# Performance work log

Measured on AMD Instinct MI355X. Metric: run time of the kernel, lower is better.

The kernel has to match this reference:

```python
import jax, jax.numpy as jnp
import numpy as np

EPS = 1e-6
TOP_K = 3
GELU_MASK_TOL = 1e-6


def _dwconv(x, w, b):
    # x: [N, C, H, W], w: [C, 1, 7, 7] depthwise (groups = C)
    y = jax.lax.conv_general_dilated(
        x, w, window_strides=(1, 1), padding=[(3, 3), (3, 3)],
        dimension_numbers=('NCHW', 'OIHW', 'NCHW'),
        feature_group_count=w.shape[0])
    if b is not None:
        y = y + b[None, :, None, None]
    return y


def _topk_pi(ph):
    # indices of top-3 |phi| along the source axis (last dim), as int16 pointers
    return jax.lax.top_k(jnp.abs(ph), TOP_K)[1].astype(jnp.int16)


def setup_inputs() -> dict:
    key = jax.random.key(0)
    ks = jax.random.split(key, 9)
    B, C, H, W, S = 1, 96, 40, 40, 100
    signal = jax.random.normal(ks[0], (B, C, H, W), jnp.float32)
    phi = jax.random.normal(ks[1], (B, C, H, W, S), jnp.float32)
    beta = jax.random.normal(ks[2], (B, C, H, W, 1), jnp.float32)
    dw_w = jax.random.normal(ks[3], (C, 1, 7, 7), jnp.float32) * 0.05
    dw_b = jax.random.normal(ks[4], (C,), jnp.float32) * 0.05
    ln_w = jnp.ones((C,), jnp.float32)
    ln_b = jnp.zeros((C,), jnp.float32)
    w1 = jax.random.normal(ks[5], (4 * C, C), jnp.float32) * (1.0 / np.sqrt(C))
    b1 = jax.random.normal(ks[6], (4 * C,), jnp.float32) * 0.05
    w2 = jax.random.normal(ks[7], (C, 4 * C), jnp.float32) * (1.0 / np.sqrt(4 * C))
    b2 = jax.random.normal(ks[8], (C,), jnp.float32) * 0.05
    gamma = jnp.full((C,), 0.01, jnp.float32)  # layer_scale_init_value
    return dict(signal=signal, phi=phi, beta=beta, dw_w=dw_w, dw_b=dw_b,
                ln_w=ln_w, ln_b=ln_b, w1=w1, b1=b1, w2=w2, b2=b2, gamma=gamma)


def reference(signal, phi, beta, dw_w, dw_b, ln_w, ln_b, w1, b1, w2, b2, gamma):
    B, C, H, W = signal.shape
    S = phi.shape[-1]

    # ---- HoloConv2d_v3 (depthwise 7x7, p=3) ----
    s = _dwconv(signal, dw_w, dw_b)
    bt = _dwconv(beta[..., 0], dw_w, dw_b)[..., None]
    ph = jnp.transpose(phi, (0, 4, 1, 2, 3)).reshape(B * S, C, H, W)
    ph = _dwconv(ph, dw_w, None).reshape(B, S, C, H, W).transpose(0, 2, 3, 4, 1)
    pi = _topk_pi(ph)

    # permute to channels_last: [B,H,W,C(,S)]
    s = s.transpose(0, 2, 3, 1)
    bt = bt.transpose(0, 2, 3, 1, 4)
    ph = ph.transpose(0, 2, 3, 1, 4)

    # ---- HoloLayerNorm_v3 (channels_last) ----
    u = s.mean(-1, keepdims=True)
    var = jnp.var(s, axis=-1, keepdims=True)  # unbiased=False
    inv = 1.0 / jnp.sqrt(var + EPS)
    scale = ln_w * inv           # [B,H,W,C]
    shift = ln_b - u * scale
    s = (s - u) * inv * ln_w + ln_b
    bt = bt * scale[..., None] + shift[..., None]
    ph = ph * scale[..., None]

    # ---- pwconv1: dim -> 4*dim (phi without bias) ----
    s = jnp.einsum('bhwc,oc->bhwo', s, w1) + b1
    bt = (jnp.einsum('bhwc,oc->bhwo', bt[..., 0], w1) + b1)[..., None]
    ph = jnp.einsum('bhwcs,oc->bhwos', ph, w1)
    pi = _topk_pi(ph)

    # ---- HoloGELU_v3 (exact erf GELU + safe ratio) ----
    g = jax.nn.gelu(s, approximate=False)
    m = jnp.abs(s) > GELU_MASK_TOL
    ratio = jnp.where(m, g / jnp.where(m, s, 1.0), 0.0)
    bt = bt * ratio[..., None]
    ph = ph * ratio[..., None]
    s = g

    # ---- pwconv2: 4*dim -> dim ----
    s = jnp.einsum('bhwo,co->bhwc', s, w2) + b2
    bt = (jnp.einsum('bhwo,co->bhwc', bt[..., 0], w2) + b2)[..., None]
    ph = jnp.einsum('bhwos,co->bhwcs', ph, w2)
    pi = _topk_pi(ph)

    # ---- layer scale ----
    s = s * gamma
    bt = bt * gamma[..., None]
    ph = ph * gamma[..., None]

    # back to channels_first + residual (pi has no residual)
    s = s.transpose(0, 3, 1, 2) + signal
    bt = bt.transpose(0, 3, 1, 2, 4) + beta
    ph = ph.transpose(0, 3, 1, 2, 4) + phi
    pi = pi.transpose(0, 3, 1, 2, 4)
    return s, ph, bt, pi
```

## Files before the change

### kernel.cpp

```cpp
#include <hip/hip_runtime.h>
#include <math.h>

#define Cc 96
#define C4 384
#define Hh 40
#define Ww 40
#define Pp 1600
#define Ss 100
#define S4 25
#define Nn 9216

#define OFF_S  0
#define OFF_PH 153600
#define OFF_BT 15513600
#define OFF_PI 15667200

#define WS_W1T   0
#define WS_W2T   36864
#define WS_RATIO 73728
#define WS_SC    WS_RATIO
#define WS_BC    (WS_RATIO + 153600)
#define WS_SCALE 688128
#define WS_RH    841728
#define WS_RM    1148928
#define WS_RL    1456128
#define WS_GH    1763328
#define WS_GM    3532800
#define WS_GL    5302272
#define WS_T     7071744
#define CHUNK    640
#define WS_NEED_CHUNK (WS_T + CHUNK*Nn)
#define WS_NEED_FULL  (WS_T + Pp*Nn)

typedef __attribute__((ext_vector_type(8))) short bf16x8_t;
typedef __attribute__((ext_vector_type(4))) float f32x4_t;

__device__ inline float4 f4fma(float4 a, float w, float4 b){
  a.x += w*b.x; a.y += w*b.y; a.z += w*b.z; a.w += w*b.w; return a;
}
__device__ inline unsigned short bf16_rne(float x){
  unsigned int u = __float_as_uint(x);
  return (unsigned short)((u + 0x7fffu + ((u>>16)&1u)) >> 16);
}
__device__ inline float bf16_to_f(unsigned short h){
  return __uint_as_float(((unsigned int)h)<<16);
}
__device__ inline void gload16(const void* g, void* l){
  __builtin_amdgcn_global_load_lds(
    (const __attribute__((address_space(1))) void*)g,
    (__attribute__((address_space(3))) void*)l, 16, 0, 0);
}

__global__ __launch_bounds__(256) void k0_transpose(const float* __restrict__ w1,
    const float* __restrict__ w2, float* __restrict__ ws){
  int idx = blockIdx.x*256 + threadIdx.x;
  if (idx < C4*Cc){
    int o = idx/Cc, c = idx%Cc;
    ws[WS_W1T + c*C4 + o] = w1[idx];
    int c2 = idx/C4, o2 = idx%C4;
    ws[WS_W2T + o2*Cc + c2] = w2[idx];
  }
}

__global__ __launch_bounds__(256) void k0g3(const float* __restrict__ w2,
    float* __restrict__ wsm){
  int i = blockIdx.x;
  int base = blockIdx.y * (Cc*C4/8);
  unsigned short* gh = (unsigned short*)(wsm + WS_GH);
  unsigned short* gm = (unsigned short*)(wsm + WS_GM);
  unsigned short* gl = (unsigned short*)(wsm + WS_GL);
  for (int k = threadIdx.x; k < Cc*C4/8; k += 256){
    int idx = base + k;
    int j = idx / C4, o = idx % C4;
    float g = w2[i*C4 + o] * wsm[WS_W1T + j*C4 + o];
    unsigned short h = bf16_rne(g);           float fh = bf16_to_f(h);
    unsigned short m = bf16_rne(g - fh);      float fm2 = bf16_to_f(m);
    unsigned short lo = bf16_rne(g - fh - fm2);
    size_t off = ((size_t)i*Cc + j)*C4 + o;
    gh[off] = h; gm[off] = m; gl[off] = lo;
  }
}

__global__ __launch_bounds__(256) void k1a_dwconv(const float* __restrict__ signal,
    const float* __restrict__ beta, const float* __restrict__ dw_w,
    const float* __restrict__ dw_b, float* __restrict__ ws){
  int c = blockIdx.x;
  int pp = blockIdx.y*256 + threadIdx.x;
  if (pp >= Pp) return;
  int h = pp / Ww, w = pp % Ww;
  float wk[49];
  #pragma unroll
  for (int i=0; i<49; i++) wk[i] = dw_w[c*49 + i];
  const float* sb = signal + (size_t)c*Pp;
  const float* bb = beta   + (size_t)c*Pp;
  float sc = 0.f, btc = 0.f;
  #pragma unroll
  for (int ky=0; ky<7; ky++){
    int y = h + ky - 3;
    if (y >= 0 && y < Hh){
      #pragma unroll
      for (int kx=0; kx<7; kx++){
        int x = w + kx - 3;
        if (x >= 0 && x < Ww){
          float wv = wk[ky*7+kx];
          sc  = fmaf(wv, sb[y*Ww + x], sc);
          btc = fmaf(wv, bb[y*Ww + x], btc);
        }
      }
    }
  }
  float b = dw_b[c];
  ws[WS_SC + (size_t)c*Pp + pp] = sc + b;
  ws[WS_BC + (size_t)c*Pp + pp] = btc + b;
}

__global__ __launch_bounds__(384) void k1_scalar(
    const float* __restrict__ signal, const float* __restrict__ beta,
    const float* __restrict__ ln_w, const float* __restrict__ ln_b,
    const float* __restrict__ b1, const float* __restrict__ b2,
    const float* __restrict__ gamma, float* __restrict__ ws,
    float* __restrict__ out){
  int p = blockIdx.x, t = threadIdx.x;
  int g = t / 96, c = t - g*96;
  __shared__ float scp[4][96], btp[4][96];
  __shared__ float sl[Cc], bl[Cc], g1[C4], g2[C4], red[2];

  float sc = 0.f, btc = 0.f;
  if (t < 96){
    sc  = ws[WS_SC + (size_t)t*Pp + p];
    btc = ws[WS_BC + (size_t)t*Pp + p];
    scp[0][t] = sc;
  }
  __syncthreads();
  if (t < 64){
    float x = scp[0][t] + (t < 32 ? scp[0][64+t] : 0.f);
    #pragma unroll
    for (int off=32; off>0; off>>=1) x += __shfl_xor(x, off);
    if (t == 0) red[0] = x * (1.f/Cc);
  }
  __syncthreads();
  float u = red[0];
  if (t < 96){ float d = sc - u; scp[1][t] = d*d; }
  __syncthreads();
  if (t < 64){
    float x = scp[1][t] + (t < 32 ? scp[1][64+t] : 0.f);
    #pragma unroll
    for (int off=32; off>0; off>>=1) x += __shfl_xor(x, off);
    if (t == 0) red[1] = x * (1.f/Cc);
  }
  __syncthreads();
  float inv = 1.0f / sqrtf(red[1] + 1e-6f);
  if (t < 96){
    float scl = ln_w[t] * inv;
    ws[WS_SCALE + p*Cc + t] = scl;
    sl[t] = (sc - u)*inv*ln_w[t] + ln_b[t];
    bl[t] = btc*scl + (ln_b[t] - u*scl);
  }
  __syncthreads();
  {
    float a = b1[t], e = b1[t];
    const float* wp = ws + WS_W1T + t;
    for (int cc=0; cc<Cc; cc++){
      float wv = wp[cc*C4];
      a = fmaf(wv, sl[cc], a);
      e = fmaf(wv, bl[cc], e);
    }
    float x = a;
    float gg = 0.5f*x*(1.f + erff(x*0.70710678118654752f));
    float r = (fabsf(x) > 1e-6f) ? gg/x : 0.f;
    unsigned short* rh = (unsigned short*)(ws + WS_RH);
    unsigned short* rm = (unsigned short*)(ws + WS_RM);
    unsigned short* rl = (unsigned short*)(ws + WS_RL);
    unsigned short hh = bf16_rne(r);          float fh = bf16_to_f(hh);
    unsigned short hm = bf16_rne(r - fh);     float fm2 = bf16_to_f(hm);
    unsigned short hl = bf16_rne(r - fh - fm2);
    rh[(size_t)p*C4 + t] = hh;
    rm[(size_t)p*C4 + t] = hm;
    rl[(size_t)p*C4 + t] = hl;
    g1[t] = gg;
    g2[t] = e*r;
  }
  __syncthreads();
  {
    float pa = 0.f, pb = 0.f;
    const float* w2p = ws + WS_W2T + (size_t)(g*96)*Cc + c;
    for (int oo=0; oo<96; oo++){
      float wv = w2p[(size_t)oo*Cc];
      pa = fmaf(wv, g1[g*96+oo], pa);
      pb = fmaf(wv, g2[g*96+oo], pb);
    }
    scp[g][c] = pa; btp[g][c] = pb;
  }
  __syncthreads();
  if (t < 96){
    float acc  = scp[0][t]+scp[1][t]+scp[2][t]+scp[3][t] + b2[t];
    float accb = btp[0][t]+btp[1][t]+btp[2][t]+btp[3][t] + b2[t];
    float gm = gamma[t];
    out[OFF_S  + t*Pp + p] = acc*gm  + signal[t*Pp + p];
    out[OFF_BT + t*Pp + p] = accb*gm + beta[t*Pp + p];
  }
}

__global__ __launch_bounds__(384) void k1_fallback(
    const float* __restrict__ signal, const float* __restrict__ beta,
    const float* __restrict__ dw_w, const float* __restrict__ dw_b,
    const float* __restrict__ ln_w, const float* __restrict__ ln_b,
    const float* __restrict__ b1, const float* __restrict__ b2,
    const float* __restrict__ gamma, float* __restrict__ ws,
    float* __restrict__ out){
  int p = blockIdx.x, t = threadIdx.x;
  int h = p / Ww, w = p % Ww;
  int g = t / 96, c = t - g*96;
  __shared__ float scp[4][96], btp[4][96];
  __shared__ float sl[Cc], bl[Cc], g1[C4], g2[C4], red[2];
  float scpart = 0.f, btpart = 0.f;
  {
    const float* wk = dw_w + c*49;
    const float* sb = signal + c*Pp;
    const float* bb = beta   + c*Pp;
    #pragma unroll
    for (int kk=0; kk<2; kk++){
      int ky = g + kk*4;
      if (ky < 7){
        int y = h + ky - 3;
        if (y >= 0 && y < Hh){
          #pragma unroll
          for (int kx=0; kx<7; kx++){
            int x = w + kx - 3;
            if (x >= 0 && x < Ww){
              float wv = wk[ky*7+kx];
              scpart  += wv * sb[y*Ww + x];
              btpart  += wv * bb[y*Ww + x];
            }
          }
        }
      }
    }
  }
  scp[g][c] = scpart; btp[g][c] = btpart;
  __syncthreads();
  float sc = 0.f, btc = 0.f;
  if (t < 96){
    sc  = scp[0][t]+scp[1][t]+scp[2][t]+scp[3][t] + dw_b[t];
    btc = btp[0][t]+btp[1][t]+btp[2][t]+btp[3][t] + dw_b[t];
    scp[0][t] = sc;
  }
  __syncthreads();
  if (t < 64){
    float x = scp[0][t] + (t < 32 ? scp[0][64+t] : 0.f);
    #pragma unroll
    for (int off=32; off>0; off>>=1) x += __shfl_xor(x, off);
    if (t == 0) red[0] = x * (1.f/Cc);
  }
  __syncthreads();
  float u = red[0];
  if (t < 96){ float d = sc - u; scp[1][t] = d*d; }
  __syncthreads();
  if (t < 64){
    float x = scp[1][t] + (t < 32 ? scp[1][64+t] : 0.f);
    #pragma unroll
    for (int off=32; off>0; off>>=1) x += __shfl_xor(x, off);
    if (t == 0) red[1] = x * (1.f/Cc);
  }
  __syncthreads();
  float inv = 1.0f / sqrtf(red[1] + 1e-6f);
  if (t < 96){
    float scl = ln_w[t] * inv;
    ws[WS_SCALE + p*Cc + t] = scl;
    sl[t] = (sc - u)*inv*ln_w[t] + ln_b[t];
    bl[t] = btc*scl + (ln_b[t] - u*scl);
  }
  __syncthreads();
  {
    float a = b1[t], e = b1[t];
    const float* wp = ws + WS_W1T + t;
    for (int cc=0; cc<Cc; cc++){
      float wv = wp[cc*C4];
      a = fmaf(wv, sl[cc], a);
      e = fmaf(wv, bl[cc], e);
    }
    float x = a;
    float gg = 0.5f*x*(1.f + erff(x*0.70710678118654752f));
    float r = (fabsf(x) > 1e-6f) ? gg/x : 0.f;
    ws[WS_RATIO + p*C4 + t] = r;
    g1[t] = gg;
    g2[t] = e*r;
  }
  __syncthreads();
  {
    float pa = 0.f, pb = 0.f;
    const float* w2p = ws + WS_W2T + (size_t)(g*96)*Cc + c;
    for (int oo=0; oo<96; oo++){
      float wv = w2p[(size_t)oo*Cc];
      pa = fmaf(wv, g1[g*96+oo], pa);
      pb = fmaf(wv, g2[g*96+oo], pb);
    }
    scp[g][c] = pa; btp[g][c] = pb;
  }
  __syncthreads();
  if (t < 96){
    float acc  = scp[0][t]+scp[1][t]+scp[2][t]+scp[3][t] + b2[t];
    float accb = btp[0][t]+btp[1][t]+btp[2][t]+btp[3][t] + b2[t];
    float gm = gamma[t];
    out[OFF_S  + t*Pp + p] = acc*gm  + signal[t*Pp + p];
    out[OFF_BT + t*Pp + p] = accb*gm + beta[t*Pp + p];
  }
}

#define STRIP 10
__global__ __launch_bounds__(256) void k2_phiconv(const float* __restrict__ phi,
    const float* __restrict__ dw_w, const float* __restrict__ wsc,
    float* __restrict__ out){
  int c = blockIdx.x;
  int task = blockIdx.y*256 + threadIdx.x;
  if (task >= Ww*S4) return;
  int w = task / S4, ss = task % S4;
  int s0 = blockIdx.z * STRIP;
  float wk[49];
  #pragma unroll
  for (int i=0; i<49; i++) wk[i] = dw_w[c*49 + i];
  const float* base = phi + (size_t)c*Pp*Ss + ss*4;
  float* ob = out + OFF_PH + (size_t)c*Pp*Ss + (size_t)w*Ss + ss*4;
  float4 z = make_float4(0.f,0.f,0.f,0.f);
  float4 a0=z,a1=z,a2=z,a3=z,a4=z,a5=z,a6=z;
  #pragma unroll
  for (int rr=0; rr<STRIP+6; rr++){
    int r = s0 - 3 + rr;
    if (r >= 0 && r < Hh){
      #pragma unroll
      for (int kx=0; kx<7; kx++){
        int x = w + kx - 3;
        if (x >= 0 && x < Ww){
          float4 in4 = *(const float4*)(base + ((size_t)r*Ww + x)*Ss);
          a0 = f4fma(a0, wk[42+kx], in4);
          a1 = f4fma(a1, wk[35+kx], in4);
          a2 = f4fma(a2, wk[28+kx], in4);
          a3 = f4fma(a3, wk[21+kx], in4);
          a4 = f4fma(a4, wk[14+kx], in4);
          a5 = f4fma(a5, wk[ 7+kx], in4);
          a6 = f4fma(a6, wk[ 0+kx], in4);
        }
      }
    }
    int hrow = r - 3;
    if (hrow >= s0 && hrow < s0 + STRIP && hrow < Hh){
      float scv = wsc[WS_SCALE + (hrow*Ww + w)*Cc + c];
      float4 o; o.x=a0.x*scv; o.y=a0.y*scv; o.z=a0.z*scv; o.w=a0.w*scv;
      *(float4*)(ob + (size_t)hrow*Ww*Ss) = o;
    }
    a0=a1; a1=a2; a2=a3; a3=a4; a4=a5; a5=a6; a6=z;
  }
}

__global__ __launch_bounds__(256) void k3g(float* __restrict__ wsm, int P0, int mtiles){
  const unsigned short* rH = (const unsigned short*)(wsm + WS_RH);
  const unsigned short* rM = (const unsigned short*)(wsm + WS_RM);
  const unsigned short* rL = (const unsigned short*)(wsm + WS_RL);
  const unsigned short* gH = (const unsigned short*)(wsm + WS_GH);
  const unsigned short* gM = (const unsigned short*)(wsm + WS_GM);
  const unsigned short* gL = (const unsigned short*)(wsm + WS_GL);
  float* tc = wsm + WS_T;

  int nblk = mtiles*72;
  int bid = blockIdx.x;
  int swz = (bid & 7)*(nblk>>3) + (bid >> 3);
  int mt = swz % mtiles, nt = swz / mtiles;
  int m0 = mt*128, n0 = nt*128;
  int t = threadIdx.x, w = t >> 6, l = t & 63;

  __shared__ __align__(16) unsigned short lds[6*4096];
  unsigned short *AH = lds,        *AM = lds+4096,  *AL = lds+8192,
                 *BH = lds+12288,  *BM = lds+16384, *BL = lds+20480;

  f32x4_t acc[4][4];
  #pragma unroll
  for (int i=0;i<4;i++)
    #pragma unroll
    for (int j=0;j<4;j++) acc[i][j] = (f32x4_t){0.f,0.f,0.f,0.f};

  int wm = (w >> 1)*64, wn = (w & 1)*64;
  int srow = w*32 + (l>>2), sbyte = (l&3)*16;
  int pA0 = P0 + m0 + srow;      if (pA0 > Pp-1) pA0 = Pp-1;
  int pA1 = P0 + m0 + srow + 16; if (pA1 > Pp-1) pA1 = Pp-1;
  int nB0 = n0 + srow, nB1 = nB0 + 16;
  int kgb = (l>>4)*16;
  int lr  = l & 15;

  for (int ks=0; ks<12; ks++){
    int k0 = ks*32;
    size_t a0o = ((size_t)pA0*C4 + k0)*2 + sbyte;
    size_t a1o = ((size_t)pA1*C4 + k0)*2 + sbyte;
    size_t b0o = ((size_t)nB0*C4 + k0)*2 + sbyte;
    size_t b1o = ((size_t)nB1*C4 + k0)*2 + sbyte;
    gload16((const char*)rH + a0o, (char*)AH + w*2048);
    gload16((const char*)rH + a1o, (char*)AH + w*2048 + 1024);
    gload16((const char*)rM + a0o, (char*)AM + w*2048);
    gload16((const char*)rM + a1o, (char*)AM + w*2048 + 1024);
    gload16((const char*)rL + a0o, (char*)AL + w*2048);
    gload16((const char*)rL + a1o, (char*)AL + w*2048 + 1024);
    gload16((const char*)gH + b0o, (char*)BH + w*2048);
    gload16((const char*)gH + b1o, (char*)BH + w*2048 + 1024);
    gload16((const char*)gM + b0o, (char*)BM + w*2048);
    gload16((const char*)gM + b1o, (char*)BM + w*2048 + 1024);
    gload16((const char*)gL + b0o, (char*)BL + w*2048);
    gload16((const char*)gL + b1o, (char*)BL + w*2048 + 1024);
    asm volatile("s_waitcnt vmcnt(0)" ::: "memory");
    __syncthreads();

    bf16x8_t aH[4], aM[4], aL[4], bHf[4], bMf[4], bLf[4];
    #pragma unroll
    for (int f=0; f<4; f++){
      int ra = (wm + f*16 + lr)*64 + kgb;
      int rb = (wn + f*16 + lr)*64 + kgb;
      aH[f]  = *(const bf16x8_t*)((const char*)AH + ra);
      aM[f]  = *(const bf16x8_t*)((const char*)AM + ra);
      aL[f]  = *(const bf16x8_t*)((const char*)AL + ra);
      bHf[f] = *(const bf16x8_t*)((const char*)BH + rb);
      bMf[f] = *(const bf16x8_t*)((const char*)BM + rb);
      bLf[f] = *(const bf16x8_t*)((const char*)BL + rb);
    }
    #pragma unroll
    for (int i=0;i<4;i++)
      #pragma unroll
      for (int j=0;j<4;j++){
        acc[i][j] = __builtin_amdgcn_mfma_f32_16x16x32_bf16(aH[i], bHf[j], acc[i][j], 0,0,0);
        acc[i][j] = __builtin_amdgcn_mfma_f32_16x16x32_bf16(aH[i], bMf[j], acc[i][j], 0,0,0);
        acc[i][j] = __builtin_amdgcn_mfma_f32_16x16x32_bf16(aM[i], bHf[j], acc[i][j], 0,0,0);
        acc[i][j] = __builtin_amdgcn_mfma_f32_16x16x32_bf16(aH[i], bLf[j], acc[i][j], 0,0,0);
        acc[i][j] = __builtin_amdgcn_mfma_f32_16x16x32_bf16(aM[i], bMf[j], acc[i][j], 0,0,0);
        acc[i][j] = __builtin_amdgcn_mfma_f32_16x16x32_bf16(aL[i], bHf[j], acc[i][j], 0,0,0);
      }
    __syncthreads();
  }

  #pragma unroll
  for (int fm=0; fm<4; fm++){
    int prow = P0 + m0 + wm + fm*16 + (l>>4)*4;
    #pragma unroll
    for (int fn=0; fn<4; fn++){
      int ncol = n0 + wn + fn*16 + lr;
      #pragma unroll
      for (int r=0; r<4; r++){
        int p = prow + r;
        if (p < Pp) tc[(size_t)(p - P0)*Nn + ncol] = acc[fm][fn][r];
      }
    }
  }
}

#define PHP 100
__global__ __launch_bounds__(512,6) void k3b_apply(const float* __restrict__ phi,
    const float* __restrict__ gamma, const float* __restrict__ wsm,
    float* __restrict__ out, int P0){
  int p = P0 + blockIdx.x, t = threadIdx.x;
  __shared__ float lp[9700];
  const float* Tg = wsm + WS_T + (size_t)blockIdx.x*Nn;
  for (int q=t; q < Cc*S4; q += 512){
    int cc = q/S4, sg = q%S4;
    *(float4*)&lp[cc*PHP + sg*4] =
      *(const float4*)(out + OFF_PH + (size_t)cc*Pp*Ss + (size_t)p*Ss + sg*4);
  }
  __syncthreads();
  int w = t >> 6, l = t & 63;
  int wu = __builtin_amdgcn_readfirstlane(w);
  const float* Tb = Tg + (size_t)wu*12*Cc;
  float2 acc[12];
  #pragma unroll
  for (int k=0;k<12;k++) acc[k] = make_float2(0.f,0.f);
  if (l < 50){
    for (int cb=0; cb<Cc; cb+=4){
      float2 pv0 = *(float2*)&lp[(cb+0)*PHP + l*2];
      float2 pv1 = *(float2*)&lp[(cb+1)*PHP + l*2];
      float2 pv2 = *(float2*)&lp[(cb+2)*PHP + l*2];
      float2 pv3 = *(float2*)&lp[(cb+3)*PHP + l*2];
      #pragma unroll
      for (int k=0;k<12;k++){
        float4 tv = *(const float4*)(Tb + k*Cc + cb);
        acc[k].x = fmaf(tv.x, pv0.x, acc[k].x);
        acc[k].y = fmaf(tv.x, pv0.y, acc[k].y);
        acc[k].x = fmaf(tv.y, pv1.x, acc[k].x);
        acc[k].y = fmaf(tv.y, pv1.y, acc[k].y);
        acc[k].x = fmaf(tv.z, pv2.x, acc[k].x);
        acc[k].y = fmaf(tv.z, pv2.y, acc[k].y);
        acc[k].x = fmaf(tv.w, pv3.x, acc[k].x);
        acc[k].y = fmaf(tv.w, pv3.y, acc[k].y);
      }
    }
    #pragma unroll
    for (int k=0;k<12;k++){
      int c = wu*12 + k;
      float gm = gamma[c];
      float2 pv = *(const float2*)(phi + (size_t)c*Pp*Ss + (size_t)p*Ss + l*2);
      float2 res;
      res.x = fmaf(acc[k].x, gm, pv.x); res.y = fmaf(acc[k].y, gm, pv.y);
      *(float2*)(out + OFF_PH + (size_t)c*Pp*Ss + (size_t)p*Ss + l*2) = res;
      acc[k].x = fabsf(acc[k].x); acc[k].y = fabsf(acc[k].y);
    }
  }
  __syncthreads();
  if (l < 50){
    #pragma unroll
    for (int k=0;k<12;k++){
      int c = wu*12 + k;
      lp[(l*2+0)*97 + c] = acc[k].x;
      lp[(l*2+1)*97 + c] = acc[k].y;
    }
  }
  __syncthreads();
  if (t < Cc){
    float v1=-1.f, v2=-1.f, v3=-1.f; int i1=0, i2=0, i3=0;
    for (int s=0; s<Ss; s++){
      float v = lp[s*97 + t];
      if (v > v1){ v3=v2;i3=i2; v2=v1;i2=i1; v1=v;i1=s; }
      else if (v > v2){ v3=v2;i3=i2; v2=v;i2=s; }
      else if (v > v3){ v3=v;i3=s; }
    }
    float* po = out + OFF_PI + (size_t)t*Pp*3 + (size_t)p*3;
    po[0] = (float)i1; po[1] = (float)i2; po[2] = (float)i3;
  }
}

__global__ __launch_bounds__(256) void k3_heavy(const float* __restrict__ phi,
     const float* __restrict__ w1, const float* __restrict__ gamma,
     const float* __restrict__ ws, float* __restrict__ out){
  int p = blockIdx.x, t = threadIdx.x;
  __shared__ float r_lds[C4];
  __shared__ float phc[Cc*Ss];
  __shared__ float Tm[Cc*Cc];
  __shared__ float pool[Cc*Ss];
  float* A1  = pool;
  float* W2s = pool + 32*Cc;
  r_lds[t] = ws[WS_RATIO + p*C4 + t];
  if (t < C4-256) r_lds[256+t] = ws[WS_RATIO + p*C4 + 256 + t];
  __syncthreads();
  for (int q=t; q < Cc*S4; q += 256){
    int cc = q/S4, s = q%S4;
    *(float4*)(phc + cc*Ss + s*4) =
      *(const float4*)(out + OFF_PH + (size_t)cc*Pp*Ss + (size_t)p*Ss + s*4);
  }
  int ti = t >> 4, tj = t & 15;
  float acc[6][6];
  #pragma unroll
  for (int k=0;k<6;k++)
    #pragma unroll
    for (int m=0;m<6;m++) acc[k][m] = 0.f;
  for (int ot=0; ot<C4; ot+=32){
    __syncthreads();
    for (int q=t; q < 32*Cc; q += 256){
      int oo = q/Cc, cc = q%Cc;
      A1[q]  = w1[(size_t)(ot+oo)*Cc + cc] * r_lds[ot+oo];
      W2s[q] = ws[WS_W2T + (ot+oo)*Cc + cc];
    }
    __syncthreads();
    #pragma unroll 4
    for (int oo=0; oo<32; oo++){
      float av[6], bv[6];
      #pragma unroll
      for (int m=0;m<6;m++) av[m] = A1[oo*Cc + tj*6 + m];
      #pragma unroll
      for (int k=0;k<6;k++) bv[k] = W2s[oo*Cc + ti*6 + k];
      #pragma unroll
      for (int k=0;k<6;k++)
        #pragma unroll
        for (int m=0;m<6;m++) acc[k][m] += bv[k]*av[m];
    }
  }
  __syncthreads();
  #pragma unroll
  for (int k=0;k<6;k++)
    #pragma unroll
    for (int m=0;m<6;m++) Tm[(ti*6+k)*Cc + tj*6 + m] = acc[k][m];
  __syncthreads();
  float* absb = pool;
  for (int q=t; q < 24*S4; q += 256){
    int cb = q/S4, s = q%S4;
    float4 z = make_float4(0.f,0.f,0.f,0.f);
    float4 o0=z, o1=z, o2=z, o3=z;
    const float* t0 = Tm + (cb*4+0)*Cc;
    const float* t1 = Tm + (cb*4+1)*Cc;
    const float* t2 = Tm + (cb*4+2)*Cc;
    const float* t3 = Tm + (cb*4+3)*Cc;
    for (int cc=0; cc<Cc; cc++){
      float4 ph4 = *(const float4*)(phc + cc*Ss + s*4);
      o0 = f4fma(o0, t0[cc], ph4);
      o1 = f4fma(o1, t1[cc], ph4);
      o2 = f4fma(o2, t2[cc], ph4);
      o3 = f4fma(o3, t3[cc], ph4);
    }
    float4 ov[4] = {o0,o1,o2,o3};
    #pragma unroll
    for (int k=0;k<4;k++){
      int c = cb*4 + k;
      float g = gamma[c];
      float4 pv = *(const float4*)(phi + (size_t)c*Pp*Ss + (size_t)p*Ss + s*4);
      float4 res;
      res.x = ov[k].x*g + pv.x; res.y = ov[k].y*g + pv.y;
      res.z = ov[k].z*g + pv.z; res.w = ov[k].w*g + pv.w;
      *(float4*)(out + OFF_PH + (size_t)c*Pp*Ss + (size_t)p*Ss + s*4) = res;
      absb[c*Ss + s*4 + 0] = fabsf(ov[k].x);
      absb[c*Ss + s*4 + 1] = fabsf(ov[k].y);
      absb[c*Ss + s*4 + 2] = fabsf(ov[k].z);
      absb[c*Ss + s*4 + 3] = fabsf(ov[k].w);
    }
  }
  __syncthreads();
  if (t < Cc){
    float v1=-1.f, v2=-1.f, v3=-1.f; int i1=0, i2=0, i3=0;
    for (int s=0; s<Ss; s++){
      float v = absb[t*Ss + s];
      if (v > v1){ v3=v2;i3=i2; v2=v1;i2=i1; v1=v;i1=s; }
      else if (v > v2){ v3=v2;i3=i2; v2=v;i2=s; }
      else if (v > v3){ v3=v;i3=s; }
    }
    float* po = out + OFF_PI + (size_t)t*Pp*3 + (size_t)p*3;
    po[0] = (float)i1; po[1] = (float)i2; po[2] = (float)i3;
  }
}

extern "C" void kernel_launch(void* const* d_in, const int* in_sizes, int n_in,
                              void* d_out, int out_size, void* d_ws, size_t ws_size,
                              hipStream_t stream){
  const float* signal = (const float*)d_in[0];
  const float* phi    = (const float*)d_in[1];
  const float* beta   = (const float*)d_in[2];
  const float* dw_w   = (const float*)d_in[3];
  const float* dw_b   = (const float*)d_in[4];
  const float* ln_w   = (const float*)d_in[5];
  const float* ln_b   = (const float*)d_in[6];
  const float* w1     = (const float*)d_in[7];
  const float* b1     = (const float*)d_in[8];
  const float* w2     = (const float*)d_in[9];
  const float* b2     = (const float*)d_in[10];
  const float* gamma  = (const float*)d_in[11];
  float* out = (float*)d_out;
  float* ws  = (float*)d_ws;

  size_t wsf = ws_size / 4;
  hipLaunchKernelGGL(k0_transpose, dim3(144), dim3(256), 0, stream, w1, w2, ws);

  if (wsf >= (size_t)WS_NEED_CHUNK){
    hipLaunchKernelGGL(k1a_dwconv, dim3(96,7), dim3(256), 0, stream,
                       signal, beta, dw_w, dw_b, ws);
    hipLaunchKernelGGL(k1_scalar, dim3(Pp), dim3(384), 0, stream,
                       signal, beta, ln_w, ln_b, b1, b2, gamma, ws, out);
  } else {
    hipLaunchKernelGGL(k1_fallback, dim3(Pp), dim3(384), 0, stream,
                       signal, beta, dw_w, dw_b, ln_w, ln_b, b1, b2, gamma, ws, out);
  }
  hipLaunchKernelGGL(k2_phiconv, dim3(96,4,4), dim3(256), 0, stream, phi, dw_w, ws, out);

  if (wsf >= (size_t)WS_NEED_FULL){
    hipLaunchKernelGGL(k0g3, dim3(Cc,8), dim3(256), 0, stream, w2, ws);
    hipLaunchKernelGGL(k3g, dim3(13*72), dim3(256), 0, stream, ws, 0, 13);
    hipLaunchKernelGGL(k3b_apply, dim3(Pp), dim3(512), 0, stream, phi, gamma, ws, out, 0);
  } else if (wsf >= (size_t)WS_NEED_CHUNK){
    hipLaunchKernelGGL(k0g3, dim3(Cc,8), dim3(256), 0, stream, w2, ws);
    for (int P0 = 0; P0 < Pp; P0 += CHUNK){
      int cp = Pp - P0; if (cp > CHUNK) cp = CHUNK;
      int mtl = (cp + 127) / 128;
      hipLaunchKernelGGL(k3g, dim3(mtl*72), dim3(256), 0, stream, ws, P0, mtl);
      hipLaunchKernelGGL(k3b_apply, dim3(cp), dim3(512), 0, stream, phi, gamma, ws, out, P0);
    }
  } else {
    hipLaunchKernelGGL(k3_heavy, dim3(Pp), dim3(256), 0, stream, phi, w1, gamma, ws, out);
  }
}
```

Measured before the change: 267.2 us.

## Read phi directly from global in k3b_apply and halve top-k LDS buffer

The apply kernel no longer stages the per-pixel phi tile in shared memory. Each lane now reads its float2 operands straight from global (strided by channel). The top-3 selection scratch shrinks from 96x100 to 48x100 floats and is processed in two passes of 48 channels, with an extra barrier inserted before the in-place writeback. Launch bounds rise from 6 to 8 blocks per CU to exploit the smaller LDS footprint. The trade-off is uncached strided global loads in the inner loop and extra synchronisation passes in exchange for higher occupancy.

```diff
diff --git a/kernel.cpp b/kernel.cpp
--- a/kernel.cpp
+++ b/kernel.cpp
@@ -448,31 +448,24 @@
   }
 }
 
-#define PHP 100
-__global__ __launch_bounds__(512,6) void k3b_apply(const float* __restrict__ phi,
+__global__ __launch_bounds__(512,8) void k3b_apply(const float* __restrict__ phi,
     const float* __restrict__ gamma, const float* __restrict__ wsm,
     float* __restrict__ out, int P0){
   int p = P0 + blockIdx.x, t = threadIdx.x;
-  __shared__ float lp[9700];
-  const float* Tg = wsm + WS_T + (size_t)blockIdx.x*Nn;
-  for (int q=t; q < Cc*S4; q += 512){
-    int cc = q/S4, sg = q%S4;
-    *(float4*)&lp[cc*PHP + sg*4] =
-      *(const float4*)(out + OFF_PH + (size_t)cc*Pp*Ss + (size_t)p*Ss + sg*4);
-  }
-  __syncthreads();
+  __shared__ float absb[100*49];
   int w = t >> 6, l = t & 63;
   int wu = __builtin_amdgcn_readfirstlane(w);
-  const float* Tb = Tg + (size_t)wu*12*Cc;
+  const float* Tb = wsm + WS_T + (size_t)blockIdx.x*Nn + (size_t)wu*12*Cc;
+  const float* phb = out + OFF_PH + (size_t)p*Ss;
   float2 acc[12];
   #pragma unroll
   for (int k=0;k<12;k++) acc[k] = make_float2(0.f,0.f);
   if (l < 50){
     for (int cb=0; cb<Cc; cb+=4){
-      float2 pv0 = *(float2*)&lp[(cb+0)*PHP + l*2];
-      float2 pv1 = *(float2*)&lp[(cb+1)*PHP + l*2];
-      float2 pv2 = *(float2*)&lp[(cb+2)*PHP + l*2];
-      float2 pv3 = *(float2*)&lp[(cb+3)*PHP + l*2];
+      float2 pv0 = *(const float2*)(phb + (size_t)(cb+0)*Pp*Ss + l*2);
+      float2 pv1 = *(const float2*)(phb + (size_t)(cb+1)*Pp*Ss + l*2);
+      float2 pv2 = *(const float2*)(phb + (size_t)(cb+2)*Pp*Ss + l*2);
+      float2 pv3 = *(const float2*)(phb + (size_t)(cb+3)*Pp*Ss + l*2);
       #pragma unroll
       for (int k=0;k<12;k++){
         float4 tv = *(const float4*)(Tb + k*Cc + cb);
@@ -486,6 +479,9 @@
         acc[k].y = fmaf(tv.w, pv3.y, acc[k].y);
       }
     }
+  }
+  __syncthreads();
+  if (l < 50){
     #pragma unroll
     for (int k=0;k<12;k++){
       int c = wu*12 + k;
@@ -497,25 +493,45 @@
       acc[k].x = fabsf(acc[k].x); acc[k].y = fabsf(acc[k].y);
     }
   }
-  __syncthreads();
-  if (l < 50){
+  if (wu < 4 && l < 50){
     #pragma unroll
     for (int k=0;k<12;k++){
       int c = wu*12 + k;
-      lp[(l*2+0)*97 + c] = acc[k].x;
-      lp[(l*2+1)*97 + c] = acc[k].y;
-    }
-  }
-  __syncthreads();
-  if (t < Cc){
+      absb[(l*2+0)*49 + c] = acc[k].x;
+      absb[(l*2+1)*49 + c] = acc[k].y;
+    }
+  }
+  __syncthreads();
+  if (t < 48){
     float v1=-1.f, v2=-1.f, v3=-1.f; int i1=0, i2=0, i3=0;
     for (int s=0; s<Ss; s++){
-      float v = lp[s*97 + t];
+      float v = absb[s*49 + t];
       if (v > v1){ v3=v2;i3=i2; v2=v1;i2=i1; v1=v;i1=s; }
       else if (v > v2){ v3=v2;i3=i2; v2=v;i2=s; }
       else if (v > v3){ v3=v;i3=s; }
     }
     float* po = out + OFF_PI + (size_t)t*Pp*3 + (size_t)p*3;
+    po[0] = (float)i1; po[1] = (float)i2; po[2] = (float)i3;
+  }
+  __syncthreads();
+  if (wu >= 4 && l < 50){
+    #pragma unroll
+    for (int k=0;k<12;k++){
+      int c = wu*12 + k - 48;
+      absb[(l*2+0)*49 + c] = acc[k].x;
+      absb[(l*2+1)*49 + c] = acc[k].y;
+    }
+  }
+  __syncthreads();
+  if (t < 48){
+    float v1=-1.f, v2=-1.f, v3=-1.f; int i1=0, i2=0, i3=0;
+    for (int s=0; s<Ss; s++){
+      float v = absb[s*49 + t];
+      if (v > v1){ v3=v2;i3=i2; v2=v1;i2=i1; v1=v;i1=s; }
+      else if (v > v2){ v3=v2;i3=i2; v2=v;i2=s; }
+      else if (v > v3){ v3=v;i3=s; }
+    }
+    float* po = out + OFF_PI + (size_t)(48+t)*Pp*3 + (size_t)p*3;
     po[0] = (float)i1; po[1] = (float)i2; po[2] = (float)i3;
   }
 }
```

Measured after the change: 283.3 us. 6.0% more time.
